# Kernel tuning notes

Measured on AMD Instinct MI355X. Metric: run time of the kernel, lower is better.

Reference implementation:

```python
import jax, jax.numpy as jnp
import numpy as np

S, B, D, H = 2048, 2, 1024, 16
DK = D // H  # 64
SCALE = 1.0 / np.sqrt(DK)


def setup_inputs() -> dict:
    key = jax.random.key(0)
    ks = jax.random.split(key, 12)
    std = 0.02
    return {
        "query": jax.random.normal(ks[0], (S, B, D), jnp.float32),
        "key": jax.random.normal(ks[1], (S, B, D), jnp.float32),
        "value": jax.random.normal(ks[2], (S, B, D), jnp.float32),
        "wq": jax.random.normal(ks[3], (D, D), jnp.float32) * std,
        "bq": jnp.zeros((D,), jnp.float32),
        "wk": jax.random.normal(ks[4], (D, D), jnp.float32) * std,
        "bk": jnp.zeros((D,), jnp.float32),
        "wv": jax.random.normal(ks[5], (D, D), jnp.float32) * std,
        "bv": jnp.zeros((D,), jnp.float32),
        "wo": jax.random.normal(ks[6], (D, D), jnp.float32) * std,
        "bo": jnp.zeros((D,), jnp.float32),
    }


def _proj(x, w, b):
    # (s, b, d_model) -> (s, b, heads, d_k); nn.Linear uses x @ W^T + b
    y = x @ w.T + b
    return y.reshape(*x.shape[:-1], H, DK)


def reference(query, key, value, wq, bq, wk, bk, wv, bv, wo, bo):
    q = _proj(query, wq, bq)   # (s, b, h, d)
    k = _proj(key, wk, bk)
    v = _proj(value, wv, bv)
    scores = jnp.einsum("ibhd,jbhd->ijbh", q, k) * SCALE  # (s_q, s_k, b, h)
    attn = jax.nn.softmax(scores, axis=1)  # softmax over key axis (dim=1)
    # dropout is identity in eval/reference mode
    x = jnp.einsum("ijbh,jbhd->ibhd", attn, v)  # (s, b, h, d)
    x = x.reshape(S, B, D)
    return x @ wo.T + bo
```

## Files before the change

kernel.cpp:

```cpp
#include <hip/hip_runtime.h>
#include <hip/hip_bf16.h>

namespace {

constexpr int SEQ = 2048;
constexpr int NB  = 2;
constexpr int DM  = 1024;
constexpr int NHD = 16;
constexpr int DKH = 64;
constexpr int MROWS = SEQ * NB;
constexpr float SM_SCALE_L2E = 0.125f * 1.44269504088896340736f;
constexpr size_t HT = (size_t)NB * NHD * SEQ * DKH;

typedef short bf16x8 __attribute__((ext_vector_type(8)));
typedef short bf16x4 __attribute__((ext_vector_type(4)));
typedef float f32x4  __attribute__((ext_vector_type(4)));

__device__ inline short f2bf(float f) {
    __hip_bfloat16 h = __float2bfloat16(f);
    return *reinterpret_cast<short*>(&h);
}

__device__ inline unsigned perm_pack_bf16(float hi, float lo) {
    return __builtin_amdgcn_perm(__float_as_uint(hi), __float_as_uint(lo),
                                 0x07060302u);
}

__device__ inline float fexp2(float x) {
#if __has_builtin(__builtin_amdgcn_exp2f)
    return __builtin_amdgcn_exp2f(x);
#else
    return exp2f(x);
#endif
}

__device__ inline void gload_lds16(const short* g, short* l) {
    __builtin_amdgcn_global_load_lds(
        (const __attribute__((address_space(1))) void*)g,
        (__attribute__((address_space(3))) void*)l, 16, 0, 0);
}

__global__ __launch_bounds__(256)
void cast_all(const float* __restrict__ q, const float* __restrict__ k,
              const float* __restrict__ v, const float* __restrict__ w0,
              const float* __restrict__ w1, const float* __restrict__ w2,
              const float* __restrict__ w3, short* __restrict__ oq,
              short* __restrict__ ok, short* __restrict__ ov,
              short* __restrict__ ow)
{
    const int y = blockIdx.y;
    const float* s;
    short* d;
    if (y < 3) {
        s = y == 0 ? q : y == 1 ? k : v;
        d = y == 0 ? oq : y == 1 ? ok : ov;
    } else {
        if (blockIdx.x >= 512) return;
        s = y == 3 ? w0 : y == 4 ? w1 : y == 5 ? w2 : w3;
        d = ow + (size_t)(y - 3) * (DM * DM);
    }
    const size_t t = (size_t)blockIdx.x * 256 + threadIdx.x;
    const float4 a = ((const float4*)s)[2 * t];
    const float4 b = ((const float4*)s)[2 * t + 1];
    short r[8] = {f2bf(a.x), f2bf(a.y), f2bf(a.z), f2bf(a.w),
                  f2bf(b.x), f2bf(b.y), f2bf(b.z), f2bf(b.w)};
    *(bf16x8*)(d + 8 * t) = *(bf16x8*)r;
}

__global__ __launch_bounds__(256)
void gemm_qkv(const short* __restrict__ X0, const short* __restrict__ X1,
              const short* __restrict__ X2, const short* __restrict__ W,
              const float* __restrict__ b0, const float* __restrict__ b1,
              const float* __restrict__ b2, short* __restrict__ Qb,
              short* __restrict__ Kb, short* __restrict__ Vt)
{
    __shared__ short sAB[2][8192];
    const int tid  = threadIdx.x;
    const int lane = tid & 63;
    const int wave = tid >> 6;
    const int i16  = lane & 15;
    const int quad = lane >> 4;

    const int c    = blockIdx.y * gridDim.x + blockIdx.x;
    const int xcd  = c & 7;
    const int idx  = c >> 3;
    const int m0   = (xcd * 4 + (idx & 3)) * 128;
    const int n0g  = (idx >> 2) * 128;

    const int R0   = (wave & 1) * 64;
    const int C0   = (wave >> 1) * 64;

    const int seg = n0g >> 10;
    const short* X = seg == 0 ? X0 : seg == 1 ? X1 : X2;

    const int rl = lane >> 2;
    const int sl = (lane & 3) ^ ((rl & 6) >> 1);

    const short* ag[2]; int alo[2];
    const short* bg[2]; int blo[2];
    #pragma unroll
    for (int i = 0; i < 2; ++i) {
        const int row = i * 64 + wave * 16 + rl;
        ag[i] = X + (size_t)(m0 + row) * DM + sl * 8;
        alo[i] = i * 2048 + wave * 512;
        bg[i] = W + (size_t)(n0g + row) * DM + sl * 8;
        blo[i] = 4096 + i * 2048 + wave * 512;
    }

    const int rsw = (quad ^ ((i16 & 6) >> 1)) * 8;
    int aoff[4], boff[4];
    #pragma unroll
    for (int rt = 0; rt < 4; ++rt)
        aoff[rt] = (R0 + rt * 16 + i16) * 32 + rsw;
    #pragma unroll
    for (int ct = 0; ct < 4; ++ct)
        boff[ct] = 4096 + (C0 + ct * 16 + i16) * 32 + rsw;

    f32x4 acc[4][4];
    #pragma unroll
    for (int rt = 0; rt < 4; ++rt)
        #pragma unroll
        for (int ct = 0; ct < 4; ++ct) acc[rt][ct] = (f32x4){0.f, 0.f, 0.f, 0.f};

    #pragma unroll
    for (int i = 0; i < 2; ++i) gload_lds16(ag[i], &sAB[0][alo[i]]);
    #pragma unroll
    for (int i = 0; i < 2; ++i) gload_lds16(bg[i], &sAB[0][blo[i]]);
    #pragma unroll
    for (int i = 0; i < 2; ++i) { ag[i] += 32; bg[i] += 32; }
    __syncthreads();

    for (int ks = 0; ks < 32; ++ks) {
        const int p = ks & 1;
        if (ks < 31) {
            #pragma unroll
            for (int i = 0; i < 2; ++i) gload_lds16(ag[i], &sAB[1 - p][alo[i]]);
            #pragma unroll
            for (int i = 0; i < 2; ++i) gload_lds16(bg[i], &sAB[1 - p][blo[i]]);
            #pragma unroll
            for (int i = 0; i < 2; ++i) { ag[i] += 32; bg[i] += 32; }
        }
        const short* buf = sAB[p];
        bf16x8 af[4], bfr[4];
        #pragma unroll
        for (int rt = 0; rt < 4; ++rt) af[rt] = *(const bf16x8*)&buf[aoff[rt]];
        #pragma unroll
        for (int ct = 0; ct < 4; ++ct) bfr[ct] = *(const bf16x8*)&buf[boff[ct]];
        #pragma unroll
        for (int rt = 0; rt < 4; ++rt)
            #pragma unroll
            for (int ct = 0; ct < 4; ++ct)
                acc[rt][ct] = __builtin_amdgcn_mfma_f32_16x16x32_bf16(
                    af[rt], bfr[ct], acc[rt][ct], 0, 0, 0);
        __syncthreads();
    }

    #pragma unroll
    for (int ct = 0; ct < 4; ++ct) {
        const int n = n0g + C0 + ct * 16 + i16;
        const int nn  = n & 1023;
        const int h = nn >> 6, dk = nn & 63;
        const float* bp = seg == 0 ? b0 : seg == 1 ? b1 : b2;
        const float bb = bp[nn];
        const float sc = seg == 0 ? SM_SCALE_L2E : 1.0f;
        #pragma unroll
        for (int rt = 0; rt < 4; ++rt)
            #pragma unroll
            for (int r = 0; r < 4; ++r) {
                const int m = m0 + R0 + rt * 16 + quad * 4 + r;
                const int s = m >> 1, b = m & 1;
                const short val = f2bf((acc[rt][ct][r] + bb) * sc);
                if (seg == 2) {
                    const int sp = (s & ~31) | (((s >> 2) & 3) << 3) |
                                   (((s >> 4) & 1) << 2) | (s & 3);
                    Vt[(((size_t)(b * NHD + h) * DKH + dk) << 11) + sp] = val;
                } else {
                    short* dst = seg == 0 ? Qb : Kb;
                    dst[((size_t)(b * NHD + h) * SEQ + s) * DKH + dk] = val;
                }
            }
    }
}

__global__ __launch_bounds__(256)
void gemm_out(const short* __restrict__ X, const short* __restrict__ W,
              const float* __restrict__ bias, float* __restrict__ Y)
{
    __shared__ short sAB[2][12288];
    const int tid  = threadIdx.x;
    const int lane = tid & 63;
    const int wave = tid >> 6;
    const int i16  = lane & 15;
    const int quad = lane >> 4;

    const int c   = blockIdx.y * gridDim.x + blockIdx.x;
    const int xcd = c & 7;
    const int idx = c >> 3;
    const int m0  = (xcd * 4 + (idx & 3)) * 128;
    const int n0  = (idx >> 2) * 64;

    const int R0   = wave * 32;

    const int srow = lane >> 3;
    const int ssl  = (lane & 7) ^ srow;

    const short* ag[4]; int alo[4];
    const short* bg[2]; int blo[2];
    #pragma unroll
    for (int i = 0; i < 4; ++i) {
        const int row = i * 32 + wave * 8 + srow;
        ag[i] = X + (size_t)(m0 + row) * DM + ssl * 8;
        alo[i] = i * 2048 + wave * 512;
    }
    #pragma unroll
    for (int i = 0; i < 2; ++i) {
        const int row = i * 32 + wave * 8 + srow;
        bg[i] = W + (size_t)(n0 + row) * DM + ssl * 8;
        blo[i] = 8192 + i * 2048 + wave * 512;
    }

    int aoff[2][2], boff[4][2];
    #pragma unroll
    for (int rt = 0; rt < 2; ++rt)
        #pragma unroll
        for (int kc = 0; kc < 2; ++kc)
            aoff[rt][kc] = (R0 + rt * 16 + i16) * 64 +
                           (((kc * 4 + quad) ^ (i16 & 7)) * 8);
    #pragma unroll
    for (int ct = 0; ct < 4; ++ct)
        #pragma unroll
        for (int kc = 0; kc < 2; ++kc)
            boff[ct][kc] = 8192 + (ct * 16 + i16) * 64 +
                           (((kc * 4 + quad) ^ (i16 & 7)) * 8);

    f32x4 acc[2][4];
    #pragma unroll
    for (int rt = 0; rt < 2; ++rt)
        #pragma unroll
        for (int ct = 0; ct < 4; ++ct) acc[rt][ct] = (f32x4){0.f, 0.f, 0.f, 0.f};

    #pragma unroll
    for (int i = 0; i < 4; ++i) gload_lds16(ag[i], &sAB[0][alo[i]]);
    #pragma unroll
    for (int i = 0; i < 2; ++i) gload_lds16(bg[i], &sAB[0][blo[i]]);
    #pragma unroll
    for (int i = 0; i < 4; ++i) ag[i] += 64;
    #pragma unroll
    for (int i = 0; i < 2; ++i) bg[i] += 64;
    __syncthreads();

    for (int ks = 0; ks < 16; ++ks) {
        const int p = ks & 1;
        if (ks < 15) {
            #pragma unroll
            for (int i = 0; i < 4; ++i) gload_lds16(ag[i], &sAB[1 - p][alo[i]]);
            #pragma unroll
            for (int i = 0; i < 2; ++i) gload_lds16(bg[i], &sAB[1 - p][blo[i]]);
            #pragma unroll
            for (int i = 0; i < 4; ++i) ag[i] += 64;
            #pragma unroll
            for (int i = 0; i < 2; ++i) bg[i] += 64;
        }
        const short* buf = sAB[p];
        #pragma unroll
        for (int kc = 0; kc < 2; ++kc) {
            bf16x8 af[2], bfr[4];
            #pragma unroll
            for (int rt = 0; rt < 2; ++rt) af[rt] = *(const bf16x8*)&buf[aoff[rt][kc]];
            #pragma unroll
            for (int ct = 0; ct < 4; ++ct) bfr[ct] = *(const bf16x8*)&buf[boff[ct][kc]];
            #pragma unroll
            for (int rt = 0; rt < 2; ++rt)
                #pragma unroll
                for (int ct = 0; ct < 4; ++ct)
                    acc[rt][ct] = __builtin_amdgcn_mfma_f32_16x16x32_bf16(
                        af[rt], bfr[ct], acc[rt][ct], 0, 0, 0);
        }
        __syncthreads();
    }

    #pragma unroll
    for (int ct = 0; ct < 4; ++ct) {
        const int n = n0 + ct * 16 + i16;
        const float bb = bias[n];
        #pragma unroll
        for (int rt = 0; rt < 2; ++rt)
            #pragma unroll
            for (int r = 0; r < 4; ++r) {
                const int m = m0 + R0 + rt * 16 + quad * 4 + r;
                Y[(size_t)m * DM + n] = acc[rt][ct][r] + bb;
            }
    }
}

__global__ __launch_bounds__(512)
void attn_mfma4(const short* __restrict__ Qb, const short* __restrict__ Kb,
                const short* __restrict__ Vtb, short* __restrict__ Xa)
{
    __shared__ short sm[32768];
    float* Of = (float*)sm;
    float* Ls = (float*)((char*)sm + 34816);

    const int tid  = threadIdx.x;
    const int lane = tid & 63;
    const int wave = tid >> 6;
    const int half = wave >> 2;
    const int w4   = wave & 3;
    const int i16  = lane & 15;
    const int quad = lane >> 4;

    const int c   = blockIdx.y * gridDim.x + blockIdx.x;
    const int xcd = c & 7;
    const int idx = c >> 3;
    const int bh  = xcd * 4 + (idx >> 4);
    const int r0  = (idx & 15) * 128;

    bf16x8 qf[2][2];
    #pragma unroll
    for (int qt = 0; qt < 2; ++qt) {
        const short* qrow =
            Qb + ((size_t)bh * SEQ + r0 + w4 * 32 + qt * 16 + i16) * DKH;
        qf[qt][0] = *(const bf16x8*)(qrow + quad * 8);
        qf[qt][1] = *(const bf16x8*)(qrow + 32 + quad * 8);
    }

    f32x4 o[2][4];
    #pragma unroll
    for (int qt = 0; qt < 2; ++qt)
        #pragma unroll
        for (int dkt = 0; dkt < 4; ++dkt) o[qt][dkt] = (f32x4){0.f, 0.f, 0.f, 0.f};
    float lsum[2] = {0.f, 0.f};

    const int srow = lane >> 3;
    const int ssl  = (lane & 7) ^ srow;
    const short* kg[2]; const short* vg[2];
    int kls[2], vls[2];
    #pragma unroll
    for (int i = 0; i < 2; ++i) {
        const int row = i * 32 + w4 * 8 + srow;
        kg[i] = Kb  + (size_t)bh * SEQ * DKH +
                (size_t)(half * 1024 + row) * DKH + ssl * 8;
        kls[i] = half * 4096 + i * 2048 + w4 * 512;
        vg[i] = Vtb + (size_t)bh * DKH * SEQ + (size_t)row * SEQ +
                half * 1024 + ssl * 8;
        vls[i] = 8192 + half * 4096 + i * 2048 + w4 * 512;
    }

    int koff[4][2];
    #pragma unroll
    for (int t = 0; t < 4; ++t)
        #pragma unroll
        for (int kc = 0; kc < 2; ++kc)
            koff[t][kc] = half * 4096 + (t * 16 + i16) * 64 +
                          (((kc * 4 + quad) ^ (i16 & 7)) * 8);
    int voff2[2][4];
    #pragma unroll
    for (int u = 0; u < 2; ++u)
        #pragma unroll
        for (int dkt = 0; dkt < 4; ++dkt)
            voff2[u][dkt] = 8192 + half * 4096 + (dkt * 16 + i16) * 64 +
                            (((u * 4 + quad) ^ (i16 & 7)) * 8);

    gload_lds16(kg[0], &sm[kls[0]]);
    gload_lds16(kg[1], &sm[kls[1]]);
    gload_lds16(vg[0], &sm[vls[0]]);
    gload_lds16(vg[1], &sm[vls[1]]);
    __syncthreads();

    for (int jt = 0; jt < 16; ++jt) {
        const int p = jt & 1;
        if (jt < 15) {
            const int bo = (1 - p) * 16384;
            gload_lds16(kg[0] + (size_t)(jt + 1) * 64 * DKH, &sm[bo + kls[0]]);
            gload_lds16(kg[1] + (size_t)(jt + 1) * 64 * DKH, &sm[bo + kls[1]]);
            gload_lds16(vg[0] + (jt + 1) * 64, &sm[bo + vls[0]]);
            gload_lds16(vg[1] + (jt + 1) * 64, &sm[bo + vls[1]]);
        }
        const short* buf = sm + p * 16384;

        bf16x8 kf[4][2];
        #pragma unroll
        for (int t = 0; t < 4; ++t) {
            kf[t][0] = *(const bf16x8*)&buf[koff[t][0]];
            kf[t][1] = *(const bf16x8*)&buf[koff[t][1]];
        }

        bf16x4 pa[2][4];
        #pragma unroll
        for (int qt = 0; qt < 2; ++qt) {
            #pragma unroll
            for (int t = 0; t < 4; ++t) {
                f32x4 st = (f32x4){0.f, 0.f, 0.f, 0.f};
                st = __builtin_amdgcn_mfma_f32_16x16x32_bf16(kf[t][0], qf[qt][0], st, 0, 0, 0);
                st = __builtin_amdgcn_mfma_f32_16x16x32_bf16(kf[t][1], qf[qt][1], st, 0, 0, 0);
                const float e0 = fexp2(st[0]);
                const float e1 = fexp2(st[1]);
                const float e2 = fexp2(st[2]);
                const float e3 = fexp2(st[3]);
                lsum[qt] += (e0 + e1) + (e2 + e3);
                union { unsigned u[2]; bf16x4 v; } pk;
                pk.u[0] = perm_pack_bf16(e1, e0);
                pk.u[1] = perm_pack_bf16(e3, e2);
                pa[qt][t] = pk.v;
            }
        }

        #pragma unroll
        for (int u = 0; u < 2; ++u) {
            const bf16x8 a0 = __builtin_shufflevector(
                pa[0][2 * u], pa[0][2 * u + 1], 0, 1, 2, 3, 4, 5, 6, 7);
            const bf16x8 a1 = __builtin_shufflevector(
                pa[1][2 * u], pa[1][2 * u + 1], 0, 1, 2, 3, 4, 5, 6, 7);
            #pragma unroll
            for (int dkt = 0; dkt < 4; ++dkt) {
                const bf16x8 vb = *(const bf16x8*)&buf[voff2[u][dkt]];
                o[0][dkt] = __builtin_amdgcn_mfma_f32_16x16x32_bf16(
                    a0, vb, o[0][dkt], 0, 0, 0);
                o[1][dkt] = __builtin_amdgcn_mfma_f32_16x16x32_bf16(
                    a1, vb, o[1][dkt], 0, 0, 0);
            }
        }
        __syncthreads();
    }

    float lred[2];
    #pragma unroll
    for (int qt = 0; qt < 2; ++qt) {
        float v = lsum[qt];
        v += __shfl_xor(v, 16, 64);
        v += __shfl_xor(v, 32, 64);
        lred[qt] = v;
    }

    if (half == 1) {
        #pragma unroll
        for (int qt = 0; qt < 2; ++qt) {
            if (quad == 0) Ls[w4 * 32 + qt * 16 + i16] = lred[qt];
            #pragma unroll
            for (int r = 0; r < 4; ++r) {
                const int row = w4 * 32 + qt * 16 + quad * 4 + r;
                #pragma unroll
                for (int dkt = 0; dkt < 4; ++dkt)
                    Of[row * 68 + dkt * 16 + i16] = o[qt][dkt][r];
            }
        }
    }
    __syncthreads();
    if (half == 0) {
        const int b = bh / NHD;
        const int h = bh % NHD;
        float linv[2];
        #pragma unroll
        for (int qt = 0; qt < 2; ++qt)
            linv[qt] = 1.f / (lred[qt] + Ls[w4 * 32 + qt * 16 + i16]);
        #pragma unroll
        for (int qt = 0; qt < 2; ++qt) {
            #pragma unroll
            for (int r = 0; r < 4; ++r) {
                const float iv = __shfl(linv[qt], quad * 4 + r, 64);
                const int row = w4 * 32 + qt * 16 + quad * 4 + r;
                const int s = r0 + row;
                const int m = s * NB + b;
                short* op = Xa + (size_t)m * DM + h * DKH;
                #pragma unroll
                for (int dkt = 0; dkt < 4; ++dkt)
                    op[dkt * 16 + i16] =
                        f2bf((o[qt][dkt][r] + Of[row * 68 + dkt * 16 + i16]) * iv);
            }
        }
    }
}

}

extern "C" void kernel_launch(void* const* d_in, const int* in_sizes, int n_in,
                              void* d_out, int out_size, void* d_ws, size_t ws_size,
                              hipStream_t stream)
{
    const float* query = (const float*)d_in[0];
    const float* key_  = (const float*)d_in[1];
    const float* value = (const float*)d_in[2];
    const float* wq    = (const float*)d_in[3];
    const float* bq    = (const float*)d_in[4];
    const float* wk    = (const float*)d_in[5];
    const float* bk    = (const float*)d_in[6];
    const float* wv    = (const float*)d_in[7];
    const float* bv    = (const float*)d_in[8];
    const float* wo    = (const float*)d_in[9];
    const float* bo    = (const float*)d_in[10];
    float* out = (float*)d_out;

    char* ws = (char*)d_ws;
    const size_t HB = HT * sizeof(short);
    short* Qb = (short*)(ws);
    short* Kb = Qb + HT;
    short* Vt = Qb + 2 * HT;
    short* Xq = (short*)(ws + 3 * HB);
    short* Xa = Xq;
    short* Xk = (short*)(ws + 4 * HB);
    short* Xv = (short*)(ws + 5 * HB);
    short* Wb = (short*)(ws + 6 * HB);

    cast_all<<<dim3(MROWS * DM / (8 * 256), 7), 256, 0, stream>>>(
        query, key_, value, wq, wk, wv, wo, Xq, Xk, Xv, Wb);

    gemm_qkv<<<dim3(MROWS / 128, 3 * DM / 128), 256, 0, stream>>>(
        Xq, Xk, Xv, Wb, bq, bk, bv, Qb, Kb, Vt);

    attn_mfma4<<<dim3(SEQ / 128, NB * NHD), 512, 0, stream>>>(Qb, Kb, Vt, Xa);

    gemm_out<<<dim3(MROWS / 128, DM / 64), 256, 0, stream>>>(
        Xa, Wb + 3 * (size_t)DM * DM, bo, out);
}
```

Measured before the change: 208.6 us.

## Triple-buffer QKV GEMM LDS staging with partial vmcnt waits

Switches the QKV projection GEMM from double to triple LDS buffering, issuing global-to-LDS loads two k-steps ahead. Each iteration waits only for the older batch of loads (vmcnt(4)) before the barrier instead of a full __syncthreads drain. The goal is to hide global load latency behind MFMA work. It raises LDS use to 48KB per block, which may reduce occupancy, and it relies on the vmcnt counting matching the four loads issued per stage.

```diff
diff --git a/kernel.cpp b/kernel.cpp
--- a/kernel.cpp
+++ b/kernel.cpp
@@ -74,7 +74,7 @@
               const float* __restrict__ b2, short* __restrict__ Qb,
               short* __restrict__ Kb, short* __restrict__ Vt)
 {
-    __shared__ short sAB[2][8192];
+    __shared__ short sAB[3][8192];
     const int tid  = threadIdx.x;
     const int lane = tid & 63;
     const int wave = tid >> 6;
@@ -122,25 +122,22 @@
         #pragma unroll
         for (int ct = 0; ct < 4; ++ct) acc[rt][ct] = (f32x4){0.f, 0.f, 0.f, 0.f};
 
-    #pragma unroll
-    for (int i = 0; i < 2; ++i) gload_lds16(ag[i], &sAB[0][alo[i]]);
-    #pragma unroll
-    for (int i = 0; i < 2; ++i) gload_lds16(bg[i], &sAB[0][blo[i]]);
-    #pragma unroll
-    for (int i = 0; i < 2; ++i) { ag[i] += 32; bg[i] += 32; }
-    __syncthreads();
+    auto stage_into = [&](short* base) {
+        gload_lds16(ag[0], base + alo[0]);
+        gload_lds16(ag[1], base + alo[1]);
+        gload_lds16(bg[0], base + blo[0]);
+        gload_lds16(bg[1], base + blo[1]);
+        ag[0] += 32; ag[1] += 32; bg[0] += 32; bg[1] += 32;
+    };
+
+    stage_into(sAB[0]);
+    stage_into(sAB[1]);
+    asm volatile("s_waitcnt vmcnt(4)" ::: "memory");
+    __builtin_amdgcn_s_barrier();
 
     for (int ks = 0; ks < 32; ++ks) {
-        const int p = ks & 1;
-        if (ks < 31) {
-            #pragma unroll
-            for (int i = 0; i < 2; ++i) gload_lds16(ag[i], &sAB[1 - p][alo[i]]);
-            #pragma unroll
-            for (int i = 0; i < 2; ++i) gload_lds16(bg[i], &sAB[1 - p][blo[i]]);
-            #pragma unroll
-            for (int i = 0; i < 2; ++i) { ag[i] += 32; bg[i] += 32; }
-        }
-        const short* buf = sAB[p];
+        if (ks < 30) stage_into(sAB[(ks + 2) % 3]);
+        const short* buf = sAB[ks % 3];
         bf16x8 af[4], bfr[4];
         #pragma unroll
         for (int rt = 0; rt < 4; ++rt) af[rt] = *(const bf16x8*)&buf[aoff[rt]];
@@ -152,7 +149,14 @@
             for (int ct = 0; ct < 4; ++ct)
                 acc[rt][ct] = __builtin_amdgcn_mfma_f32_16x16x32_bf16(
                     af[rt], bfr[ct], acc[rt][ct], 0, 0, 0);
-        __syncthreads();
+        if (ks < 31) {
+            if (ks < 30) {
+                asm volatile("s_waitcnt vmcnt(4)" ::: "memory");
+            } else {
+                asm volatile("s_waitcnt vmcnt(0)" ::: "memory");
+            }
+            __builtin_amdgcn_s_barrier();
+        }
     }
 
     #pragma unroll
```

Result: no change. 210.6 us (+0.9%).

## Drop split-KV in attention; each block handles 256 queries over full key range

Applied to the files above, without the earlier changes.

The attention kernel no longer splits the key sequence between two halves of the block with an LDS reduction at the end. Each of the 8 waves now owns 32 query rows across all 2048 keys, so a block covers 256 queries and the grid is halved. K/V tiles are shared by all waves, which halves LDS use and removes the final cross-half merge and its barrier, at the cost of fewer blocks and a longer serial loop per block. The QKV GEMM k-loop is also fully unrolled, with load addresses computed from the loop index instead of incremented pointers.

```diff
diff --git a/kernel.cpp b/kernel.cpp
--- a/kernel.cpp
+++ b/kernel.cpp
@@ -122,23 +122,20 @@
         #pragma unroll
         for (int ct = 0; ct < 4; ++ct) acc[rt][ct] = (f32x4){0.f, 0.f, 0.f, 0.f};
 
-    #pragma unroll
-    for (int i = 0; i < 2; ++i) gload_lds16(ag[i], &sAB[0][alo[i]]);
-    #pragma unroll
-    for (int i = 0; i < 2; ++i) gload_lds16(bg[i], &sAB[0][blo[i]]);
-    #pragma unroll
-    for (int i = 0; i < 2; ++i) { ag[i] += 32; bg[i] += 32; }
+    gload_lds16(ag[0], &sAB[0][alo[0]]);
+    gload_lds16(ag[1], &sAB[0][alo[1]]);
+    gload_lds16(bg[0], &sAB[0][blo[0]]);
+    gload_lds16(bg[1], &sAB[0][blo[1]]);
     __syncthreads();
 
+    #pragma unroll
     for (int ks = 0; ks < 32; ++ks) {
         const int p = ks & 1;
         if (ks < 31) {
-            #pragma unroll
-            for (int i = 0; i < 2; ++i) gload_lds16(ag[i], &sAB[1 - p][alo[i]]);
-            #pragma unroll
-            for (int i = 0; i < 2; ++i) gload_lds16(bg[i], &sAB[1 - p][blo[i]]);
-            #pragma unroll
-            for (int i = 0; i < 2; ++i) { ag[i] += 32; bg[i] += 32; }
+            gload_lds16(ag[0] + (ks + 1) * 32, &sAB[1 - p][alo[0]]);
+            gload_lds16(ag[1] + (ks + 1) * 32, &sAB[1 - p][alo[1]]);
+            gload_lds16(bg[0] + (ks + 1) * 32, &sAB[1 - p][blo[0]]);
+            gload_lds16(bg[1] + (ks + 1) * 32, &sAB[1 - p][blo[1]]);
         }
         const short* buf = sAB[p];
         bf16x8 af[4], bfr[4];
@@ -297,29 +294,25 @@
 void attn_mfma4(const short* __restrict__ Qb, const short* __restrict__ Kb,
                 const short* __restrict__ Vtb, short* __restrict__ Xa)
 {
-    __shared__ short sm[32768];
-    float* Of = (float*)sm;
-    float* Ls = (float*)((char*)sm + 34816);
+    __shared__ short sm[16384];
 
     const int tid  = threadIdx.x;
     const int lane = tid & 63;
     const int wave = tid >> 6;
-    const int half = wave >> 2;
-    const int w4   = wave & 3;
     const int i16  = lane & 15;
     const int quad = lane >> 4;
 
     const int c   = blockIdx.y * gridDim.x + blockIdx.x;
     const int xcd = c & 7;
     const int idx = c >> 3;
-    const int bh  = xcd * 4 + (idx >> 4);
-    const int r0  = (idx & 15) * 128;
+    const int bh  = xcd * 4 + (idx & 3);
+    const int r0  = (idx >> 2) * 256;
 
     bf16x8 qf[2][2];
     #pragma unroll
     for (int qt = 0; qt < 2; ++qt) {
         const short* qrow =
-            Qb + ((size_t)bh * SEQ + r0 + w4 * 32 + qt * 16 + i16) * DKH;
+            Qb + ((size_t)bh * SEQ + r0 + wave * 32 + qt * 16 + i16) * DKH;
         qf[qt][0] = *(const bf16x8*)(qrow + quad * 8);
         qf[qt][1] = *(const bf16x8*)(qrow + 32 + quad * 8);
     }
@@ -333,50 +326,40 @@
 
     const int srow = lane >> 3;
     const int ssl  = (lane & 7) ^ srow;
-    const short* kg[2]; const short* vg[2];
-    int kls[2], vls[2];
-    #pragma unroll
-    for (int i = 0; i < 2; ++i) {
-        const int row = i * 32 + w4 * 8 + srow;
-        kg[i] = Kb  + (size_t)bh * SEQ * DKH +
-                (size_t)(half * 1024 + row) * DKH + ssl * 8;
-        kls[i] = half * 4096 + i * 2048 + w4 * 512;
-        vg[i] = Vtb + (size_t)bh * DKH * SEQ + (size_t)row * SEQ +
-                half * 1024 + ssl * 8;
-        vls[i] = 8192 + half * 4096 + i * 2048 + w4 * 512;
-    }
+    const short* kg = Kb  + (size_t)bh * SEQ * DKH +
+                      (size_t)(wave * 8 + srow) * DKH + ssl * 8;
+    const short* vg = Vtb + (size_t)bh * DKH * SEQ +
+                      (size_t)(wave * 8 + srow) * SEQ + ssl * 8;
+    const int kls = wave * 512;
+    const int vls = 4096 + wave * 512;
 
     int koff[4][2];
     #pragma unroll
     for (int t = 0; t < 4; ++t)
         #pragma unroll
         for (int kc = 0; kc < 2; ++kc)
-            koff[t][kc] = half * 4096 + (t * 16 + i16) * 64 +
+            koff[t][kc] = (t * 16 + i16) * 64 +
                           (((kc * 4 + quad) ^ (i16 & 7)) * 8);
     int voff2[2][4];
     #pragma unroll
     for (int u = 0; u < 2; ++u)
         #pragma unroll
         for (int dkt = 0; dkt < 4; ++dkt)
-            voff2[u][dkt] = 8192 + half * 4096 + (dkt * 16 + i16) * 64 +
+            voff2[u][dkt] = 4096 + (dkt * 16 + i16) * 64 +
                             (((u * 4 + quad) ^ (i16 & 7)) * 8);
 
-    gload_lds16(kg[0], &sm[kls[0]]);
-    gload_lds16(kg[1], &sm[kls[1]]);
-    gload_lds16(vg[0], &sm[vls[0]]);
-    gload_lds16(vg[1], &sm[vls[1]]);
+    gload_lds16(kg, &sm[kls]);
+    gload_lds16(vg, &sm[vls]);
     __syncthreads();
 
-    for (int jt = 0; jt < 16; ++jt) {
+    for (int jt = 0; jt < 32; ++jt) {
         const int p = jt & 1;
-        if (jt < 15) {
-            const int bo = (1 - p) * 16384;
-            gload_lds16(kg[0] + (size_t)(jt + 1) * 64 * DKH, &sm[bo + kls[0]]);
-            gload_lds16(kg[1] + (size_t)(jt + 1) * 64 * DKH, &sm[bo + kls[1]]);
-            gload_lds16(vg[0] + (jt + 1) * 64, &sm[bo + vls[0]]);
-            gload_lds16(vg[1] + (jt + 1) * 64, &sm[bo + vls[1]]);
-        }
-        const short* buf = sm + p * 16384;
+        if (jt < 31) {
+            const int bo = (1 - p) * 8192;
+            gload_lds16(kg + (size_t)(jt + 1) * 64 * DKH, &sm[bo + kls]);
+            gload_lds16(vg + (jt + 1) * 64, &sm[bo + vls]);
+        }
+        const short* buf = sm + p * 8192;
 
         bf16x8 kf[4][2];
         #pragma unroll
@@ -423,50 +406,28 @@
         __syncthreads();
     }
 
-    float lred[2];
+    float linv[2];
     #pragma unroll
     for (int qt = 0; qt < 2; ++qt) {
         float v = lsum[qt];
         v += __shfl_xor(v, 16, 64);
         v += __shfl_xor(v, 32, 64);
-        lred[qt] = v;
-    }
-
-    if (half == 1) {
-        #pragma unroll
-        for (int qt = 0; qt < 2; ++qt) {
-            if (quad == 0) Ls[w4 * 32 + qt * 16 + i16] = lred[qt];
-            #pragma unroll
-            for (int r = 0; r < 4; ++r) {
-                const int row = w4 * 32 + qt * 16 + quad * 4 + r;
-                #pragma unroll
-                for (int dkt = 0; dkt < 4; ++dkt)
-                    Of[row * 68 + dkt * 16 + i16] = o[qt][dkt][r];
-            }
-        }
-    }
-    __syncthreads();
-    if (half == 0) {
-        const int b = bh / NHD;
-        const int h = bh % NHD;
-        float linv[2];
-        #pragma unroll
-        for (int qt = 0; qt < 2; ++qt)
-            linv[qt] = 1.f / (lred[qt] + Ls[w4 * 32 + qt * 16 + i16]);
-        #pragma unroll
-        for (int qt = 0; qt < 2; ++qt) {
-            #pragma unroll
-            for (int r = 0; r < 4; ++r) {
-                const float iv = __shfl(linv[qt], quad * 4 + r, 64);
-                const int row = w4 * 32 + qt * 16 + quad * 4 + r;
-                const int s = r0 + row;
-                const int m = s * NB + b;
-                short* op = Xa + (size_t)m * DM + h * DKH;
-                #pragma unroll
-                for (int dkt = 0; dkt < 4; ++dkt)
-                    op[dkt * 16 + i16] =
-                        f2bf((o[qt][dkt][r] + Of[row * 68 + dkt * 16 + i16]) * iv);
-            }
+        linv[qt] = 1.f / v;
+    }
+    const int b = bh / NHD;
+    const int h = bh % NHD;
+    #pragma unroll
+    for (int qt = 0; qt < 2; ++qt) {
+        #pragma unroll
+        for (int r = 0; r < 4; ++r) {
+            const float iv = __shfl(linv[qt], quad * 4 + r, 64);
+            const int row = wave * 32 + qt * 16 + quad * 4 + r;
+            const int s = r0 + row;
+            const int m = s * NB + b;
+            short* op = Xa + (size_t)m * DM + h * DKH;
+            #pragma unroll
+            for (int dkt = 0; dkt < 4; ++dkt)
+                op[dkt * 16 + i16] = f2bf(o[qt][dkt][r] * iv);
         }
     }
 }
@@ -507,7 +468,7 @@
     gemm_qkv<<<dim3(MROWS / 128, 3 * DM / 128), 256, 0, stream>>>(
         Xq, Xk, Xv, Wb, bq, bk, bv, Qb, Kb, Vt);
 
-    attn_mfma4<<<dim3(SEQ / 128, NB * NHD), 512, 0, stream>>>(Qb, Kb, Vt, Xa);
+    attn_mfma4<<<dim3(SEQ / 256, NB * NHD), 512, 0, stream>>>(Qb, Kb, Vt, Xa);
 
     gemm_out<<<dim3(MROWS / 128, DM / 64), 256, 0, stream>>>(
         Xa, Wb + 3 * (size_t)DM * DM, bo, out);
```

After: 201.7 us. 3.3% less time.
